# Optimization experiments

Measured on AMD Instinct MI355X. Metric: run time of the kernel, lower is better.

## Reference

```python
import jax, jax.numpy as jnp
import numpy as np

N_FEATURES = 256
HIDDEN = 16
BATCH = 32768


def setup_inputs() -> dict:
    key = jax.random.key(0)
    ks = jax.random.split(key, 8)
    F, H = N_FEATURES, HIDDEN
    x = jax.random.normal(ks[0], (BATCH, F), dtype=jnp.float32)
    # Stacked per-feature subnet params (torch Linear: y = x @ W.T + b)
    s1 = 1.0  # fan_in=1 for fc1
    W1 = jax.random.uniform(ks[1], (F, H), minval=-s1, maxval=s1, dtype=jnp.float32)
    b1 = jax.random.uniform(ks[2], (F, H), minval=-s1, maxval=s1, dtype=jnp.float32)
    s2 = 1.0 / np.sqrt(H)
    W2 = jax.random.uniform(ks[3], (F, H, H), minval=-s2, maxval=s2, dtype=jnp.float32)  # [F, out, in]
    b2 = jax.random.uniform(ks[4], (F, H), minval=-s2, maxval=s2, dtype=jnp.float32)
    W3 = jax.random.uniform(ks[5], (F, H), minval=-s2, maxval=s2, dtype=jnp.float32)  # out=1
    b3 = jax.random.uniform(ks[6], (F,), minval=-s2, maxval=s2, dtype=jnp.float32)
    linear_a = jnp.zeros((F,), dtype=jnp.float32)
    bias_b = jnp.zeros((1,), dtype=jnp.float32)
    return {"x": x, "linear_a": linear_a, "bias_b": bias_b,
            "W1": W1, "b1": b1, "W2": W2, "b2": b2, "W3": W3, "b3": b3}


def reference(x, linear_a, bias_b, W1, b1, W2, b2, W3, b3):
    # lin term: (x * a).sum(1)
    lin = x @ linear_a  # [B]
    # all subnets batched: h1 [B, F, H]
    h1 = jax.nn.relu(x[:, :, None] * W1[None, :, :] + b1[None, :, :])
    # fc2: y = h1 @ W2.T per feature; W2 is [F, out, in]
    h2 = jax.nn.relu(jnp.einsum('bfh,fkh->bfk', h1, W2) + b2[None, :, :])
    # fc3 -> scalar per feature, then sum over features
    out_f = jnp.einsum('bfh,fh->bf', h2, W3) + b3[None, :]  # [B, F]
    add_sum = out_f.sum(axis=1)  # [B]
    logits = lin + bias_b[0] + add_sum
    return logits
```

## Files before the change

### kernel.cpp

```cpp
#include <hip/hip_runtime.h>


typedef float    f32x4 __attribute__((ext_vector_type(4)));
typedef _Float16 f16x4 __attribute__((ext_vector_type(4)));
typedef __fp16   pk16x2 __attribute__((ext_vector_type(2)));

__device__ __forceinline__ f16x4 cvt4(f32x4 v) {
    pk16x2 lo = __builtin_amdgcn_cvt_pkrtz(v[0], v[1]);
    pk16x2 hi = __builtin_amdgcn_cvt_pkrtz(v[2], v[3]);
    union { unsigned u[2]; f16x4 h; } un;
    un.u[0] = __builtin_bit_cast(unsigned, lo);
    un.u[1] = __builtin_bit_cast(unsigned, hi);
    return un.h;
}

__device__ __forceinline__ f16x4 relu_h(f16x4 v) {
    f16x4 z = {};
    return __builtin_elementwise_max(v, z);
}

__device__ __forceinline__ f32x4 relu_f(f32x4 v) {
    f32x4 z = {0.f, 0.f, 0.f, 0.f};
    return __builtin_elementwise_max(v, z);
}

#define FCHUNK 16
#define XR     20
#define W2R    20

__global__ __launch_bounds__(256) void igann_kernel(
    const float* __restrict__ x,  const float* __restrict__ la,
    const float* __restrict__ bb, const float* __restrict__ W1,
    const float* __restrict__ b1, const float* __restrict__ W2,
    const float* __restrict__ b2, const float* __restrict__ W3,
    const float* __restrict__ b3, float* __restrict__ out)
{
    const int tid = threadIdx.x;
    const int l   = tid & 63;
    const int w   = tid >> 6;
    const int r   = l & 15;
    const int g   = l >> 4;
    const int g4  = g * 4;

    const int rb = blockIdx.x >> 4;
    const int fg = blockIdx.x & 15;
    const int f0 = fg * FCHUNK;
    const int rowbase = rb * 256;

    __shared__ _Float16 xs [256 * XR];
    __shared__ _Float16 w2s[FCHUNK * 16 * W2R];
    __shared__ _Float16 w1s[FCHUNK * 16];
    __shared__ _Float16 b1s[FCHUNK * 16];
    __shared__ float    b2s[FCHUNK * 16];
    __shared__ float    w3s[FCHUNK * 16];
    __shared__ float    red[256];

    {
        const int rr = tid >> 2;
        const int c4 = (tid & 3) * 4;
        #pragma unroll
        for (int it = 0; it < 4; ++it) {
            const int row = it * 64 + rr;
            f32x4 v = *(const f32x4*)(x + (size_t)(rowbase + row) * 256 + f0 + c4);
            *(f16x4*)(xs + row * XR + c4) = cvt4(v);
        }
    }
    {
        const int f = tid >> 4, n = tid & 15;
        const float* src = W2 + ((size_t)(f0 + f) * 16 + n) * 16;
        _Float16* dst = w2s + (f * 16 + n) * W2R;
        #pragma unroll
        for (int q = 0; q < 4; ++q) {
            f32x4 v = *(const f32x4*)(src + q * 4);
            *(f16x4*)(dst + q * 4) = cvt4(v);
        }
    }
    w1s[tid] = (_Float16)W1[f0 * 16 + tid];
    b1s[tid] = (_Float16)b1[f0 * 16 + tid];
    b2s[tid] = b2[f0 * 16 + tid];
    w3s[tid] = W3[f0 * 16 + tid];
    __syncthreads();

    const _Float16* xw = xs + (w * 64 + r) * XR;

    f32x4 acc[4];
    #pragma unroll
    for (int t = 0; t < 4; ++t) acc[t] = (f32x4){0.f, 0.f, 0.f, 0.f};

    for (int fi = 0; fi < FCHUNK; fi += 4) {
        f16x4 xv[4];
        #pragma unroll
        for (int t = 0; t < 4; ++t)
            xv[t] = *(const f16x4*)(xw + t * 16 * XR + fi);

        #pragma unroll
        for (int u = 0; u < 4; ++u) {
            const int f = fi + u;
            f16x4 w1h   = *(const f16x4*)(w1s + f * 16 + g4);
            f16x4 b1h   = *(const f16x4*)(b1s + f * 16 + g4);
            f16x4 bfrag = *(const f16x4*)(w2s + (f * 16 + r) * W2R + g4);
            const float b2k = b2s[f * 16 + r];
            const float w3k = w3s[f * 16 + r];
            const f32x4 cinit = {b2k, b2k, b2k, b2k};
            const f32x4 w3k4  = {w3k, w3k, w3k, w3k};

            #pragma unroll
            for (int t = 0; t < 4; ++t) {
                const _Float16 s = xv[t][u];
                f16x4 xb = {s, s, s, s};
                f16x4 h = relu_h(xb * w1h + b1h);
                f32x4 d = __builtin_amdgcn_mfma_f32_16x16x16f16(h, bfrag, cinit, 0, 0, 0);
                acc[t] += relu_f(d) * w3k4;
            }
        }
    }

    #pragma unroll
    for (int t = 0; t < 4; ++t)
        #pragma unroll
        for (int j = 0; j < 4; ++j) {
            float v = acc[t][j];
            v += __shfl_xor(v, 1, 64);
            v += __shfl_xor(v, 2, 64);
            v += __shfl_xor(v, 4, 64);
            v += __shfl_xor(v, 8, 64);
            if (r == 0) red[w * 64 + t * 16 + g4 + j] = v;
        }
    __syncthreads();

    float lin = 0.f, b3s = 0.f;
    const _Float16* xrow = xs + tid * XR;
    #pragma unroll
    for (int c = 0; c < FCHUNK; ++c) {
        lin = fmaf((float)xrow[c], la[f0 + c], lin);
        b3s += b3[f0 + c];
    }
    const float v = red[tid] + lin + b3s + (fg == 0 ? bb[0] : 0.f);
    atomicAdd(out + rowbase + tid, v);
}

extern "C" void kernel_launch(void* const* d_in, const int* in_sizes, int n_in,
                              void* d_out, int out_size, void* d_ws, size_t ws_size,
                              hipStream_t stream) {
    const float* x  = (const float*)d_in[0];
    const float* la = (const float*)d_in[1];
    const float* bb = (const float*)d_in[2];
    const float* W1 = (const float*)d_in[3];
    const float* b1 = (const float*)d_in[4];
    const float* W2 = (const float*)d_in[5];
    const float* b2 = (const float*)d_in[6];
    const float* W3 = (const float*)d_in[7];
    const float* b3 = (const float*)d_in[8];
    float* out = (float*)d_out;

    (void)hipMemsetAsync(out, 0, (size_t)out_size * sizeof(float), stream);

    dim3 grid(2048), block(256);
    hipLaunchKernelGGL(igann_kernel, grid, block, 0, stream,
                       x, la, bb, W1, b1, W2, b2, W3, b3, out);
}
```

Before: 108.9 us.

## Load x directly into registers with prefetch, drop LDS staging and reduction barrier

Removes the shared-memory staging of the x tile and instead has each lane load its own row values from global memory straight into registers, prefetching the next four features while computing the current ones. The linear term is now computed from full-precision registers. The shared reduction buffer and its second barrier are replaced by direct atomic adds from the shuffle-reduced lanes plus a separate atomic for the linear term and constants. This doubles the number of atomics per row and uses uncoalesced 16-byte strided global loads in place of cooperative coalesced loads.

```diff
diff --git a/kernel.cpp b/kernel.cpp
--- a/kernel.cpp
+++ b/kernel.cpp
@@ -25,8 +25,6 @@
 }
 
 #define FCHUNK 16
-#define XR     20
-#define W2R    20
 
 __global__ __launch_bounds__(256) void igann_kernel(
     const float* __restrict__ x,  const float* __restrict__ la,
@@ -47,28 +45,16 @@
     const int f0 = fg * FCHUNK;
     const int rowbase = rb * 256;
 
-    __shared__ _Float16 xs [256 * XR];
-    __shared__ _Float16 w2s[FCHUNK * 16 * W2R];
+    __shared__ _Float16 w2s[FCHUNK * 16 * 16];
     __shared__ _Float16 w1s[FCHUNK * 16];
     __shared__ _Float16 b1s[FCHUNK * 16];
     __shared__ float    b2s[FCHUNK * 16];
     __shared__ float    w3s[FCHUNK * 16];
-    __shared__ float    red[256];
 
-    {
-        const int rr = tid >> 2;
-        const int c4 = (tid & 3) * 4;
-        #pragma unroll
-        for (int it = 0; it < 4; ++it) {
-            const int row = it * 64 + rr;
-            f32x4 v = *(const f32x4*)(x + (size_t)(rowbase + row) * 256 + f0 + c4);
-            *(f16x4*)(xs + row * XR + c4) = cvt4(v);
-        }
-    }
     {
         const int f = tid >> 4, n = tid & 15;
         const float* src = W2 + ((size_t)(f0 + f) * 16 + n) * 16;
-        _Float16* dst = w2s + (f * 16 + n) * W2R;
+        _Float16* dst = w2s + (f * 16 + n) * 16;
         #pragma unroll
         for (int q = 0; q < 4; ++q) {
             f32x4 v = *(const f32x4*)(src + q * 4);
@@ -81,24 +67,45 @@
     w3s[tid] = W3[f0 * 16 + tid];
     __syncthreads();
 
-    const _Float16* xw = xs + (w * 64 + r) * XR;
+    float b3s = 0.f;
+    #pragma unroll
+    for (int c = 0; c < FCHUNK; ++c) b3s += b3[f0 + c];
+    const float gconst = b3s + (fg == 0 ? bb[0] : 0.f);
+
+    const float* xbase = x + (size_t)(rowbase + w * 64 + r) * 256 + f0;
 
     f32x4 acc[4];
+    float lin[4];
     #pragma unroll
-    for (int t = 0; t < 4; ++t) acc[t] = (f32x4){0.f, 0.f, 0.f, 0.f};
+    for (int t = 0; t < 4; ++t) { acc[t] = (f32x4){0.f, 0.f, 0.f, 0.f}; lin[t] = 0.f; }
+
+    f32x4 xf[4], xn[4];
+    #pragma unroll
+    for (int t = 0; t < 4; ++t)
+        xf[t] = *(const f32x4*)(xbase + t * 16 * 256);
 
     for (int fi = 0; fi < FCHUNK; fi += 4) {
-        f16x4 xv[4];
+        if (fi < FCHUNK - 4) {
+            #pragma unroll
+            for (int t = 0; t < 4; ++t)
+                xn[t] = *(const f32x4*)(xbase + t * 16 * 256 + fi + 4);
+        }
+        f16x4 xh[4];
+        #pragma unroll
+        for (int t = 0; t < 4; ++t) xh[t] = cvt4(xf[t]);
+
         #pragma unroll
         for (int t = 0; t < 4; ++t)
-            xv[t] = *(const f16x4*)(xw + t * 16 * XR + fi);
+            #pragma unroll
+            for (int c = 0; c < 4; ++c)
+                lin[t] = fmaf(xf[t][c], la[f0 + fi + c], lin[t]);
 
         #pragma unroll
         for (int u = 0; u < 4; ++u) {
             const int f = fi + u;
             f16x4 w1h   = *(const f16x4*)(w1s + f * 16 + g4);
             f16x4 b1h   = *(const f16x4*)(b1s + f * 16 + g4);
-            f16x4 bfrag = *(const f16x4*)(w2s + (f * 16 + r) * W2R + g4);
+            f16x4 bfrag = *(const f16x4*)(w2s + (f * 16 + r) * 16 + g4);
             const float b2k = b2s[f * 16 + r];
             const float w3k = w3s[f * 16 + r];
             const f32x4 cinit = {b2k, b2k, b2k, b2k};
@@ -106,12 +113,16 @@
 
             #pragma unroll
             for (int t = 0; t < 4; ++t) {
-                const _Float16 s = xv[t][u];
+                const _Float16 s = xh[t][u];
                 f16x4 xb = {s, s, s, s};
                 f16x4 h = relu_h(xb * w1h + b1h);
                 f32x4 d = __builtin_amdgcn_mfma_f32_16x16x16f16(h, bfrag, cinit, 0, 0, 0);
                 acc[t] += relu_f(d) * w3k4;
             }
+        }
+        if (fi < FCHUNK - 4) {
+            #pragma unroll
+            for (int t = 0; t < 4; ++t) xf[t] = xn[t];
         }
     }
 
@@ -124,19 +135,15 @@
             v += __shfl_xor(v, 2, 64);
             v += __shfl_xor(v, 4, 64);
             v += __shfl_xor(v, 8, 64);
-            if (r == 0) red[w * 64 + t * 16 + g4 + j] = v;
+            if (r == 0)
+                atomicAdd(out + rowbase + w * 64 + t * 16 + g4 + j, v);
         }
-    __syncthreads();
 
-    float lin = 0.f, b3s = 0.f;
-    const _Float16* xrow = xs + tid * XR;
-    #pragma unroll
-    for (int c = 0; c < FCHUNK; ++c) {
-        lin = fmaf((float)xrow[c], la[f0 + c], lin);
-        b3s += b3[f0 + c];
+    if (g == 0) {
+        #pragma unroll
+        for (int t = 0; t < 4; ++t)
+            atomicAdd(out + rowbase + w * 64 + t * 16 + r, lin[t] + gconst);
     }
-    const float v = red[tid] + lin + b3s + (fg == 0 ? bb[0] : 0.f);
-    atomicAdd(out + rowbase + tid, v);
 }
 
 extern "C" void kernel_launch(void* const* d_in, const int* in_sizes, int n_in,
```

Result: slower. 113.9 us (+4.7%).
